# Performance work log

Hardware: AMD Instinct MI355X
Metric: run time of the kernel (lower is better)

## Reference

```python
import jax, jax.numpy as jnp
import numpy as np
from jax import lax

EPS = 1e-5
SLOPE = 0.01  # default leaky_relu negative slope

def _conv1d(x, w):
    # x: [B, Cin, L], w: [Cout, Cin, K]; padding=1 (same for K=3)
    return lax.conv_general_dilated(x, w, window_strides=(1,), padding=[(1, 1)],
                                    dimension_numbers=('NCH', 'OIH', 'NCH'))

def _bn_train(x, gamma, beta, axes):
    # training-mode BatchNorm: batch stats over `axes`, biased variance
    mean = jnp.mean(x, axis=axes, keepdims=True)
    var = jnp.mean(jnp.square(x - mean), axis=axes, keepdims=True)
    shape = [1] * x.ndim
    shape[1] = x.shape[1]
    g = gamma.reshape(shape); b = beta.reshape(shape)
    return (x - mean) * g / jnp.sqrt(var + EPS) + b

def setup_inputs() -> dict:
    key = jax.random.key(0)
    ks = jax.random.split(key, 6)
    d, d2, out_dim = 64, 128, 128
    bs, T, N = 16, 32, 256
    s = 0.05
    return {
        'x': jax.random.normal(ks[0], (bs, T, N, d), jnp.float32),
        'conv1_w': jax.random.normal(ks[1], (d2, d, 3), jnp.float32) * s,
        'bn1_g': jnp.ones((d2,), jnp.float32), 'bn1_b': jnp.zeros((d2,), jnp.float32),
        'conv2_w': jax.random.normal(ks[2], (d2, d2, 3), jnp.float32) * s,
        'bn2_g': jnp.ones((d2,), jnp.float32), 'bn2_b': jnp.zeros((d2,), jnp.float32),
        'map_w': jax.random.normal(ks[3], (d2, d2), jnp.float32) * s,
        'map_b': jnp.zeros((d2,), jnp.float32),
        'theta_w': jax.random.normal(ks[4], (out_dim, d2), jnp.float32) * s,
        'theta_b': jnp.zeros((out_dim,), jnp.float32),
        'bnS_g': jnp.ones((out_dim,), jnp.float32), 'bnS_b': jnp.zeros((out_dim,), jnp.float32),
    }

def reference(x, conv1_w, bn1_g, bn1_b, conv2_w, bn2_g, bn2_b,
              map_w, map_b, theta_w, theta_b, bnS_g, bnS_b):
    bs, T, N, d = x.shape
    d2 = 2 * d
    # ---- Temporal 1D CNN over time, per node ----
    tem = jnp.transpose(x, (0, 2, 1, 3)).reshape(bs * N, T, d)      # [BN, T, d]
    h = jnp.transpose(tem, (0, 2, 1))                               # [BN, d, T]
    h = jax.nn.relu(_bn_train(_conv1d(h, conv1_w), bn1_g, bn1_b, (0, 2)))
    h = jax.nn.relu(_bn_train(_conv1d(h, conv2_w), bn2_g, bn2_b, (0, 2)))  # [BN, 2d, T]
    # faithful raw reshape (mixes channel/time layout exactly like the torch code)
    tem_out = h.reshape(bs, N, T, d2)
    spa = jnp.transpose(tem_out, (0, 2, 1, 3)).reshape(bs * T, N, d2)  # [B', N, 2d]
    # ---- Dot-product graph construction ----
    mapped = jnp.einsum('bnd,ed->bne', spa, map_w) + map_b            # Linear(2d,2d)
    adj = jnp.einsum('bnd,bmd->bnm', mapped, mapped)                  # [B', N, N]
    eye = jnp.eye(N, dtype=adj.dtype)
    adj = jax.nn.leaky_relu(adj - eye * 1e8, SLOPE)
    adj = jax.nn.softmax(adj, axis=-1) + eye
    # ---- MPNN (k=1): theta(A @ X), BN over channels, leaky_relu ----
    agg = jnp.einsum('bnm,bmd->bnd', adj, spa)                        # bmm(A, X)
    out = jnp.einsum('bnd,od->bno', agg, theta_w) + theta_b           # [B', N, out]
    out = jnp.transpose(out, (0, 2, 1))                               # [B', out, N]
    out = _bn_train(out, bnS_g, bnS_b, (0, 2))
    out = jnp.transpose(out, (0, 2, 1))
    return jax.nn.leaky_relu(out, SLOPE)
```

## Files before the change

### kernel.cpp

```cpp
#include <hip/hip_runtime.h>

#define SLOPE 0.01f
#define EPSB 1e-5f
#define INV_CNT (1.0f/131072.0f)

typedef unsigned short u16;
typedef unsigned int u32;
typedef __attribute__((ext_vector_type(8))) short s16x8;
typedef __attribute__((ext_vector_type(4))) float f4;

__device__ float g_stats[3][2][128];
__device__ float g_sb[3][2][128];
__device__ float g_part[2048][256];
__device__ u16 g_w1h[3][128][64];
__device__ u16 g_w1l[3][128][64];
__device__ u16 g_w2h[3][128][128];
__device__ u16 g_w2l[3][128][128];
__device__ u16 g_wmh[128][128];
__device__ u16 g_wml[128][128];
__device__ u16 g_wqh[128][128];
__device__ u16 g_wql[128][128];

__device__ __forceinline__ float lrelu(float x){ return x > 0.f ? x : SLOPE*x; }
__device__ __forceinline__ u16 f2b(float f){
  u32 u = __float_as_uint(f);
  return (u16)((u + 0x7fffu + ((u >> 16) & 1u)) >> 16);
}
__device__ __forceinline__ float b2f(u16 h){ return __uint_as_float(((u32)h) << 16); }
__device__ __forceinline__ u32 pk(float a, float b){ return (u32)f2b(a) | ((u32)f2b(b) << 16); }
__device__ __forceinline__ u32 pkhl(float f){
  u16 h = f2b(f);
  u16 l = f2b(f - b2f(h));
  return (u32)h | ((u32)l << 16);
}
__device__ __forceinline__ float unhl(u32 v){ return b2f((u16)(v & 0xffff)) + b2f((u16)(v >> 16)); }

__global__ void k_zero(){
  int i = blockIdx.x*256 + threadIdx.x;
  if (i < 768) ((float*)g_stats)[i] = 0.f;
}

__global__ void k_reduce(int which){
  const float* base = &g_part[blockIdx.x*128][0];
  int j = threadIdx.x;
  float s = 0.f;
  #pragma unroll 4
  for (int r = 0; r < 128; ++r) s += base[r*256 + j];
  atomicAdd(&((float*)g_stats)[which*256 + j], s);
}

__global__ void k_prepw(const float* __restrict__ w1, const float* __restrict__ w2,
                        const float* __restrict__ mapw, const float* __restrict__ thw){
  int idx = blockIdx.x*256 + threadIdx.x;
  if (idx < 24576){
    int kk = idx >> 13, r = idx & 8191, co = r >> 6, ci = r & 63;
    float v = w1[co*192 + ci*3 + kk];
    u16 h = f2b(v);
    g_w1h[kk][co][ci] = h; g_w1l[kk][co][ci] = f2b(v - b2f(h));
  } else if (idx < 73728){
    int j = idx - 24576;
    int kk = j >> 14, r = j & 16383, co = r >> 7, ci = r & 127;
    float v = w2[co*384 + ci*3 + kk];
    u16 h = f2b(v);
    g_w2h[kk][co][ci] = h; g_w2l[kk][co][ci] = f2b(v - b2f(h));
  } else if (idx < 90112){
    int j = idx - 73728;
    float v = mapw[j];
    u16 h = f2b(v);
    ((u16*)g_wmh)[j] = h; ((u16*)g_wml)[j] = f2b(v - b2f(h));
  } else if (idx < 106496){
    int j = idx - 90112;
    float v = thw[j];
    u16 h = f2b(v);
    ((u16*)g_wqh)[j] = h; ((u16*)g_wql)[j] = f2b(v - b2f(h));
  }
}

__global__ void k_finalize(const float* __restrict__ g, const float* __restrict__ bta, int which){
  int c = threadIdx.x;
  float mean = g_stats[which][0][c] * INV_CNT;
  float var  = g_stats[which][1][c] * INV_CNT - mean*mean;
  float sc = g[c] * rsqrtf(var + EPSB);
  g_sb[which][0][c] = sc;
  g_sb[which][1][c] = bta[c] - mean*sc;
}

__global__ __launch_bounds__(256, 4) void k_conv1(const float* __restrict__ x, u16* __restrict__ y1hl){
  __shared__ __align__(16) u16 a0h[2][34][72];
  __shared__ __align__(16) u16 a0l[2][34][72];
  const int bid = blockIdx.x;
  const int bn0 = bid*2;
  const int b = bn0 >> 8, n = bn0 & 255;
  const int tid = threadIdx.x;
  const int w = tid >> 6, l = tid & 63, quad = l >> 4, lm = l & 15;
  f4 acc[2][4];
  #pragma unroll
  for (int i = 0; i < 2; ++i)
    #pragma unroll
    for (int j = 0; j < 4; ++j) acc[i][j] = (f4)0.f;

  {
    int nn = tid >> 7, rem = tid & 127, t = rem >> 2, ci0 = (rem & 3)*16;
    const float* px = x + ((b*32 + t)*256 + n + nn)*64 + ci0;
    u16 hh[16], ll[16];
    #pragma unroll
    for (int j = 0; j < 4; ++j){
      float4 v = *(const float4*)(px + 4*j);
      float vv[4] = {v.x, v.y, v.z, v.w};
      #pragma unroll
      for (int e = 0; e < 4; ++e){
        u16 h = f2b(vv[e]);
        hh[4*j+e] = h; ll[4*j+e] = f2b(vv[e] - b2f(h));
      }
    }
    *(uint4*)&a0h[nn][t+1][ci0]   = *(uint4*)&hh[0];
    *(uint4*)&a0h[nn][t+1][ci0+8] = *(uint4*)&hh[8];
    *(uint4*)&a0l[nn][t+1][ci0]   = *(uint4*)&ll[0];
    *(uint4*)&a0l[nn][t+1][ci0+8] = *(uint4*)&ll[8];
  }
  for (int u = tid; u < 288; u += 256){
    int a = u / 144, rr = u % 144, r = rr / 36, cw = rr % 36;
    u32* base = a ? (u32*)&a0l[r>>1][(r&1)*33][0] : (u32*)&a0h[r>>1][(r&1)*33][0];
    base[cw] = 0u;
  }
  __syncthreads();

  for (int kk = 0; kk < 3; ++kk){
    #pragma unroll
    for (int s = 0; s < 2; ++s){
      int ci0 = s*32 + quad*8;
      s16x8 wh[2], wl[2], bh[4], bl[4];
      #pragma unroll
      for (int i = 0; i < 2; ++i){
        wh[i] = *(const s16x8*)&g_w1h[kk][(2*w+i)*16 + lm][ci0];
        wl[i] = *(const s16x8*)&g_w1l[kk][(2*w+i)*16 + lm][ci0];
      }
      #pragma unroll
      for (int nt = 0; nt < 4; ++nt){
        bh[nt] = *(s16x8*)&a0h[nt>>1][(nt&1)*16 + lm + kk][ci0];
        bl[nt] = *(s16x8*)&a0l[nt>>1][(nt&1)*16 + lm + kk][ci0];
      }
      #pragma unroll
      for (int i = 0; i < 2; ++i)
        #pragma unroll
        for (int nt = 0; nt < 4; ++nt){
          acc[i][nt] = __builtin_amdgcn_mfma_f32_16x16x32_bf16(wh[i], bh[nt], acc[i][nt], 0, 0, 0);
          acc[i][nt] = __builtin_amdgcn_mfma_f32_16x16x32_bf16(wh[i], bl[nt], acc[i][nt], 0, 0, 0);
          acc[i][nt] = __builtin_amdgcn_mfma_f32_16x16x32_bf16(wl[i], bh[nt], acc[i][nt], 0, 0, 0);
        }
    }
  }
  #pragma unroll
  for (int i = 0; i < 2; ++i){
    int co0 = (2*w+i)*16 + quad*4;
    float s0=0,s1=0,s2=0,s3=0,q0=0,q1=0,q2=0,q3=0;
    #pragma unroll
    for (int nt = 0; nt < 4; ++nt){
      f4 a = acc[i][nt];
      int nn = nt >> 1, t = (nt & 1)*16 + lm;
      uint4 p;
      p.x = pkhl(a.x); p.y = pkhl(a.y); p.z = pkhl(a.z); p.w = pkhl(a.w);
      *(uint4*)&y1hl[(((bn0+nn)*32 + t)*128 + co0)*2] = p;
      s0+=a.x; s1+=a.y; s2+=a.z; s3+=a.w;
      q0+=a.x*a.x; q1+=a.y*a.y; q2+=a.z*a.z; q3+=a.w*a.w;
    }
    #pragma unroll
    for (int m = 1; m < 16; m <<= 1){
      s0+=__shfl_xor(s0,m); s1+=__shfl_xor(s1,m); s2+=__shfl_xor(s2,m); s3+=__shfl_xor(s3,m);
      q0+=__shfl_xor(q0,m); q1+=__shfl_xor(q1,m); q2+=__shfl_xor(q2,m); q3+=__shfl_xor(q3,m);
    }
    if (lm == 0){
      f4 sv = {s0,s1,s2,s3}, qv = {q0,q1,q2,q3};
      *(f4*)&g_part[bid][co0]       = sv;
      *(f4*)&g_part[bid][128 + co0] = qv;
    }
  }
}

__global__ __launch_bounds__(256, 4) void k_conv2(const u16* __restrict__ y1hl, u16* __restrict__ spa){
  __shared__ __align__(16) u16 a1s[2][34][136];
  const int bid = blockIdx.x;
  const int bn0 = bid*2;
  const int b = bn0 >> 8, n = bn0 & 255;
  const int tid = threadIdx.x;
  const int w = tid >> 6, l = tid & 63, quad = l >> 4, lm = l & 15;
  f4 acc2[4][2];
  #pragma unroll
  for (int mt = 0; mt < 4; ++mt)
    #pragma unroll
    for (int i = 0; i < 2; ++i) acc2[mt][i] = (f4)0.f;

  {
    int nn = tid >> 7, rem = tid & 127, t = rem >> 2, ci0 = (rem & 3)*32;
    const u16* py = y1hl + (((bn0+nn)*32 + t)*128)*2;
    #pragma unroll
    for (int j = 0; j < 4; ++j){
      uint4 va = *(const uint4*)&py[(ci0 + 8*j)*2];
      uint4 vb = *(const uint4*)&py[(ci0 + 8*j + 4)*2];
      u32 vv[8] = {va.x, va.y, va.z, va.w, vb.x, vb.y, vb.z, vb.w};
      u16 oo[8];
      #pragma unroll
      for (int e = 0; e < 8; ++e){
        int ci = ci0 + 8*j + e;
        float f = fmaxf(fmaf(unhl(vv[e]), g_sb[0][0][ci], g_sb[0][1][ci]), 0.f);
        oo[e] = f2b(f);
      }
      *(uint4*)&a1s[nn][t+1][ci0 + 8*j] = *(uint4*)&oo[0];
    }
  }
  for (int u = tid; u < 272; u += 256){
    int r = u/68, cw = u%68;
    ((u32*)&a1s[r>>1][(r&1)*33][0])[cw] = 0u;
  }
  __syncthreads();

  for (int kk = 0; kk < 3; ++kk){
    #pragma unroll
    for (int s = 0; s < 4; ++s){
      int ci0 = s*32 + quad*8;
      s16x8 ax[4], bwh[2], bwl[2];
      #pragma unroll
      for (int i = 0; i < 2; ++i){
        bwh[i] = *(const s16x8*)&g_w2h[kk][(2*w+i)*16 + lm][ci0];
        bwl[i] = *(const s16x8*)&g_w2l[kk][(2*w+i)*16 + lm][ci0];
      }
      #pragma unroll
      for (int mt = 0; mt < 4; ++mt) ax[mt] = *(s16x8*)&a1s[mt>>1][(mt&1)*16 + lm + kk][ci0];
      #pragma unroll
      for (int mt = 0; mt < 4; ++mt)
        #pragma unroll
        for (int i = 0; i < 2; ++i){
          acc2[mt][i] = __builtin_amdgcn_mfma_f32_16x16x32_bf16(ax[mt], bwh[i], acc2[mt][i], 0, 0, 0);
          acc2[mt][i] = __builtin_amdgcn_mfma_f32_16x16x32_bf16(ax[mt], bwl[i], acc2[mt][i], 0, 0, 0);
        }
    }
  }
  #pragma unroll
  for (int i = 0; i < 2; ++i){
    int co = (2*w+i)*16 + lm;
    float s = 0.f, q = 0.f;
    #pragma unroll
    for (int mt = 0; mt < 4; ++mt){
      f4 a = acc2[mt][i];
      int off0 = co*32 + (mt&1)*16 + quad*4;
      int tp = off0 >> 7, cp = off0 & 127;
      int row = (b*32 + tp)*256 + (n + (mt>>1));
      uint2 p; p.x = pk(a.x, a.y); p.y = pk(a.z, a.w);
      *(uint2*)&spa[row*128 + cp] = p;
      s += a.x + a.y + a.z + a.w;
      q += a.x*a.x + a.y*a.y + a.z*a.z + a.w*a.w;
    }
    s += __shfl_xor(s, 16); s += __shfl_xor(s, 32);
    q += __shfl_xor(q, 16); q += __shfl_xor(q, 32);
    if (l < 16){
      g_part[bid][co]       = s;
      g_part[bid][128 + co] = q;
    }
  }
}

__global__ __launch_bounds__(256, 4) void k_gemm128b(const u16* A,
                                                     u16* spaw,
                                                     const float* __restrict__ bvec,
                                                     void* __restrict__ outv,
                                                     int wsel, int do_stats){
  __shared__ __align__(16) u16 As[64][136];
  const u16* Wh = wsel ? &g_wqh[0][0] : &g_wmh[0][0];
  const u16* Wl = wsel ? &g_wql[0][0] : &g_wml[0][0];
  const int bid = blockIdx.x;
  const int rowbase = bid * 64;
  const int tid = threadIdx.x;
  const int w = tid >> 6, l = tid & 63, quad = l >> 4, lm = l & 15;
  f4 acc[2][4];
  #pragma unroll
  for (int i = 0; i < 2; ++i)
    #pragma unroll
    for (int rt = 0; rt < 4; ++rt) acc[i][rt] = (f4)0.f;

  { int r = tid >> 2, c0 = (tid & 3)*32;
    int row = rowbase + r;
    if (wsel == 0){
      int c = ((row >> 8) & 31)*4 + (tid & 3);
      float sc = g_sb[1][0][c], bi = g_sb[1][1][c];
      #pragma unroll
      for (int j = 0; j < 4; ++j){
        uint4 v = *(const uint4*)&A[row*128 + c0 + 8*j];
        u32 vv[4] = {v.x, v.y, v.z, v.w};
        u16 oo[8];
        #pragma unroll
        for (int e = 0; e < 4; ++e){
          oo[2*e]   = f2b(fmaxf(fmaf(b2f((u16)(vv[e] & 0xffff)), sc, bi), 0.f));
          oo[2*e+1] = f2b(fmaxf(fmaf(b2f((u16)(vv[e] >> 16)),    sc, bi), 0.f));
        }
        uint4 ov = *(uint4*)&oo[0];
        *(uint4*)&As[r][c0 + 8*j] = ov;
        *(uint4*)&spaw[row*128 + c0 + 8*j] = ov;
      }
    } else {
      #pragma unroll
      for (int j = 0; j < 4; ++j)
        *(uint4*)&As[r][c0 + 8*j] = *(const uint4*)&A[row*128 + c0 + 8*j];
    }
  }
  __syncthreads();

  #pragma unroll
  for (int s = 0; s < 4; ++s){
    int k0 = s*32 + quad*8;
    s16x8 awh[2], awl[2], ba[4];
    #pragma unroll
    for (int i = 0; i < 2; ++i){
      awh[i] = *(const s16x8*)&Wh[((2*w+i)*16 + lm)*128 + k0];
      awl[i] = *(const s16x8*)&Wl[((2*w+i)*16 + lm)*128 + k0];
    }
    #pragma unroll
    for (int rt = 0; rt < 4; ++rt) ba[rt] = *(s16x8*)&As[rt*16 + lm][k0];
    #pragma unroll
    for (int i = 0; i < 2; ++i)
      #pragma unroll
      for (int rt = 0; rt < 4; ++rt){
        acc[i][rt] = __builtin_amdgcn_mfma_f32_16x16x32_bf16(awh[i], ba[rt], acc[i][rt], 0, 0, 0);
        acc[i][rt] = __builtin_amdgcn_mfma_f32_16x16x32_bf16(awl[i], ba[rt], acc[i][rt], 0, 0, 0);
      }
  }
  #pragma unroll
  for (int i = 0; i < 2; ++i){
    int e0 = (2*w+i)*16 + quad*4;
    f4 bv = *(const f4*)&bvec[e0];
    if (wsel == 0){
      u16* mh = (u16*)outv;
      u16* ml = mh + 16777216;
      int dc = e0 >> 5, ec = e0 & 31;
      #pragma unroll
      for (int rt = 0; rt < 4; ++rt){
        int row = rowbase + rt*16 + lm;
        int bp = row >> 8, m = row & 255;
        f4 o = acc[i][rt] + bv;
        float fv[4] = {o.x, o.y, o.z, o.w};
        u16 hh[4], ll[4];
        #pragma unroll
        for (int e = 0; e < 4; ++e){
          u16 h = f2b(fv[e]);
          hh[e] = h; ll[e] = f2b(fv[e] - b2f(h));
        }
        int off = ((bp*4 + dc)*256 + m)*32 + ec;
        *(uint2*)&mh[off] = *(uint2*)&hh[0];
        *(uint2*)&ml[off] = *(uint2*)&ll[0];
      }
    } else {
      float* outp = (float*)outv;
      f4 sv = (f4)0.f, qv = (f4)0.f;
      #pragma unroll
      for (int rt = 0; rt < 4; ++rt){
        int row = rowbase + rt*16 + lm;
        f4 o = acc[i][rt] + bv;
        *(f4*)&outp[row*128 + e0] = o;
        sv += o; qv += o*o;
      }
      if (do_stats){
        #pragma unroll
        for (int m = 1; m < 16; m <<= 1){
          sv.x+=__shfl_xor(sv.x,m); sv.y+=__shfl_xor(sv.y,m); sv.z+=__shfl_xor(sv.z,m); sv.w+=__shfl_xor(sv.w,m);
          qv.x+=__shfl_xor(qv.x,m); qv.y+=__shfl_xor(qv.y,m); qv.z+=__shfl_xor(qv.z,m); qv.w+=__shfl_xor(qv.w,m);
        }
        if (lm == 0){
          *(f4*)&g_part[bid][e0]       = sv;
          *(f4*)&g_part[bid][128 + e0] = qv;
        }
      }
    }
  }
}

__global__ __launch_bounds__(256) void k_adjagg(const u16* __restrict__ mh,
                                                const u16* __restrict__ ml,
                                                const u16* __restrict__ spa,
                                                u16* __restrict__ agg){
  __shared__ __align__(16) char smem[52224];
  u16 (*mbh)[40]   = (u16(*)[40])(smem);
  u16 (*mbl)[40]   = (u16(*)[40])(smem + 20480);
  u16 (*Ps)[264]   = (u16(*)[264])(smem);
  u16 (*spasT)[72] = (u16(*)[72])(smem + 33792);
  const int rb = blockIdx.x;
  const int vb = (rb & 7)*256 + (rb >> 3);
  const int bp = vb >> 2;
  const int nt = vb & 3;
  const int tid = threadIdx.x;
  const int w = tid >> 6, l = tid & 63, quad = l >> 4, lm = l & 15;

  f4 sacc[16];
  #pragma unroll
  for (int ct = 0; ct < 16; ++ct) sacc[ct] = (f4)0.f;

  for (int dc = 0; dc < 4; ++dc){
    __syncthreads();
    {
      const u16* srch = mh + ((bp*4 + dc) << 13);
      const u16* srcl = ml + ((bp*4 + dc) << 13);
      int m0 = tid >> 2, seg = (tid & 3)*8;
      #pragma unroll
      for (int r = 0; r < 4; ++r){
        int m = m0 + r*64;
        *(uint4*)&mbh[m][seg] = *(const uint4*)&srch[m*32 + seg];
        *(uint4*)&mbl[m][seg] = *(const uint4*)&srcl[m*32 + seg];
      }
    }
    __syncthreads();
    s16x8 amh = *(s16x8*)&mbh[nt*64 + w*16 + lm][quad*8];
    s16x8 aml = *(s16x8*)&mbl[nt*64 + w*16 + lm][quad*8];
    #pragma unroll
    for (int ct = 0; ct < 16; ++ct){
      s16x8 bmh = *(s16x8*)&mbh[ct*16 + lm][quad*8];
      s16x8 bml = *(s16x8*)&mbl[ct*16 + lm][quad*8];
      sacc[ct] = __builtin_amdgcn_mfma_f32_16x16x32_bf16(amh, bmh, sacc[ct], 0, 0, 0);
      sacc[ct] = __builtin_amdgcn_mfma_f32_16x16x32_bf16(amh, bml, sacc[ct], 0, 0, 0);
      sacc[ct] = __builtin_amdgcn_mfma_f32_16x16x32_bf16(aml, bmh, sacc[ct], 0, 0, 0);
    }
  }
  __syncthreads();

  #pragma unroll
  for (int r = 0; r < 4; ++r){
    int rowg = nt*64 + w*16 + quad*4 + r;
    float v[16]; float mx = -3.0e38f;
    #pragma unroll
    for (int ct = 0; ct < 16; ++ct){
      float t = sacc[ct][r];
      if (ct*16 + lm == rowg) t -= 1e8f;
      t = lrelu(t);
      v[ct] = t; mx = fmaxf(mx, t);
    }
    #pragma unroll
    for (int m = 1; m < 16; m <<= 1) mx = fmaxf(mx, __shfl_xor(mx, m));
    float sum = 0.f;
    #pragma unroll
    for (int ct = 0; ct < 16; ++ct){ float e = __expf(v[ct] - mx); v[ct] = e; sum += e; }
    #pragma unroll
    for (int m = 1; m < 16; m <<= 1) sum += __shfl_xor(sum, m);
    float inv = 1.0f / sum;
    #pragma unroll
    for (int ct = 0; ct < 16; ++ct)
      Ps[w*16 + quad*4 + r][ct*16 + lm] = f2b(v[ct] * inv);
  }

  f4 acc2[2][4];
  #pragma unroll
  for (int i = 0; i < 2; ++i)
    #pragma unroll
    for (int rt = 0; rt < 4; ++rt) acc2[i][rt] = (f4)0.f;

  for (int mc2 = 0; mc2 < 4; ++mc2){
    __syncthreads();
    {
      int mlo = tid & 63;
      int db = (tid >> 6)*8;
      const u16* ps = spa + (bp*256 + mc2*64 + mlo)*128;
      #pragma unroll
      for (int r = 0; r < 4; ++r){
        int d0 = db + r*32;
        uint4 v = *(const uint4*)(ps + d0);
        u16 h[8]; *(uint4*)&h[0] = v;
        #pragma unroll
        for (int j = 0; j < 8; ++j) spasT[d0+j][mlo] = h[j];
      }
    }
    __syncthreads();
    #pragma unroll
    for (int ks = 0; ks < 2; ++ks){
      int m0 = ks*32 + quad*8;
      s16x8 afs[2], bfp[4];
      #pragma unroll
      for (int i = 0; i < 2; ++i) afs[i] = *(s16x8*)&spasT[(2*w+i)*16 + lm][m0];
      #pragma unroll
      for (int rt = 0; rt < 4; ++rt) bfp[rt] = *(s16x8*)&Ps[rt*16 + lm][mc2*64 + m0];
      #pragma unroll
      for (int i = 0; i < 2; ++i)
        #pragma unroll
        for (int rt = 0; rt < 4; ++rt)
          acc2[i][rt] = __builtin_amdgcn_mfma_f32_16x16x32_bf16(afs[i], bfp[rt], acc2[i][rt], 0, 0, 0);
    }
  }
  #pragma unroll
  for (int i = 0; i < 2; ++i){
    int d0 = (2*w+i)*16 + quad*4;
    #pragma unroll
    for (int rt = 0; rt < 4; ++rt){
      int grow = bp*256 + nt*64 + rt*16 + lm;
      uint2 sp = *(const uint2*)&spa[grow*128 + d0];
      f4 a = acc2[i][rt];
      a.x += b2f((u16)(sp.x & 0xffff)); a.y += b2f((u16)(sp.x >> 16));
      a.z += b2f((u16)(sp.y & 0xffff)); a.w += b2f((u16)(sp.y >> 16));
      uint2 p; p.x = pk(a.x, a.y); p.y = pk(a.z, a.w);
      *(uint2*)&agg[grow*128 + d0] = p;
    }
  }
}

__global__ void k_bnout(float* __restrict__ outp){
  int idx = blockIdx.x*256 + threadIdx.x;
  int flat = idx*4;
  int o = flat & 127;
  float4 v = *(const float4*)(outp + flat);
  v.x = lrelu(fmaf(v.x, g_sb[2][0][o+0], g_sb[2][1][o+0]));
  v.y = lrelu(fmaf(v.y, g_sb[2][0][o+1], g_sb[2][1][o+1]));
  v.z = lrelu(fmaf(v.z, g_sb[2][0][o+2], g_sb[2][1][o+2]));
  v.w = lrelu(fmaf(v.w, g_sb[2][0][o+3], g_sb[2][1][o+3]));
  *(float4*)(outp + flat) = v;
}

extern "C" void kernel_launch(void* const* d_in, const int* in_sizes, int n_in,
                              void* d_out, int out_size, void* d_ws, size_t ws_size,
                              hipStream_t stream) {
  const float* x    = (const float*)d_in[0];
  const float* w1   = (const float*)d_in[1];
  const float* bn1g = (const float*)d_in[2];
  const float* bn1b = (const float*)d_in[3];
  const float* w2   = (const float*)d_in[4];
  const float* bn2g = (const float*)d_in[5];
  const float* bn2b = (const float*)d_in[6];
  const float* mapw = (const float*)d_in[7];
  const float* mapb = (const float*)d_in[8];
  const float* thw  = (const float*)d_in[9];
  const float* thb  = (const float*)d_in[10];
  const float* bnSg = (const float*)d_in[11];
  const float* bnSb = (const float*)d_in[12];
  float* outp = (float*)d_out;

  u16* spa = (u16*)d_ws;
  u16* agg = spa + 16777216;

  u16* y1hl = (u16*)d_out;
  u16* mh   = (u16*)d_out;
  u16* ml   = mh + 16777216;

  k_zero<<<3, 256, 0, stream>>>();
  k_prepw<<<416, 256, 0, stream>>>(w1, w2, mapw, thw);
  k_conv1<<<2048, 256, 0, stream>>>(x, y1hl);
  k_reduce<<<16, 256, 0, stream>>>(0);
  k_finalize<<<1, 128, 0, stream>>>(bn1g, bn1b, 0);
  k_conv2<<<2048, 256, 0, stream>>>(y1hl, spa);
  k_reduce<<<16, 256, 0, stream>>>(1);
  k_finalize<<<1, 128, 0, stream>>>(bn2g, bn2b, 1);
  k_gemm128b<<<2048, 256, 0, stream>>>(spa, spa, mapb, (void*)mh, 0, 0);
  k_adjagg<<<2048, 256, 0, stream>>>(mh, ml, spa, agg);
  k_gemm128b<<<2048, 256, 0, stream>>>(agg, agg, thb, (void*)outp, 1, 1);
  k_reduce<<<16, 256, 0, stream>>>(2);
  k_finalize<<<1, 128, 0, stream>>>(bnSg, bnSb, 2);
  k_bnout<<<16384, 256, 0, stream>>>(outp);
}
```

Before: 406.2 us.

## Fuse BN reductions with finalize, store conv1 output as fp32, pretranspose spa

Folds k_zero into k_prepw and merges k_finalize into k_reduce with a last-block counter, removing four kernel launches. Conv1 now writes plain fp32 instead of packed hi/lo bf16 pairs, which keeps the same byte count but drops the split and recombine arithmetic. The mapping GEMM also writes a transposed copy of spa into a global buffer, so adjagg can load spasT with vector copies instead of doing an element-wise transpose in shared memory. The cost is an extra 32 MB scattered 2-byte write in the GEMM.

```diff
diff --git a/kernel.cpp b/kernel.cpp
--- a/kernel.cpp
+++ b/kernel.cpp
@@ -12,6 +12,7 @@
 __device__ float g_stats[3][2][128];
 __device__ float g_sb[3][2][128];
 __device__ float g_part[2048][256];
+__device__ int   g_cnt[3];
 __device__ u16 g_w1h[3][128][64];
 __device__ u16 g_w1l[3][128][64];
 __device__ u16 g_w2h[3][128][128];
@@ -20,6 +21,7 @@
 __device__ u16 g_wml[128][128];
 __device__ u16 g_wqh[128][128];
 __device__ u16 g_wql[128][128];
+__device__ u16 g_sT[16777216];
 
 __device__ __forceinline__ float lrelu(float x){ return x > 0.f ? x : SLOPE*x; }
 __device__ __forceinline__ u16 f2b(float f){
@@ -28,30 +30,12 @@
 }
 __device__ __forceinline__ float b2f(u16 h){ return __uint_as_float(((u32)h) << 16); }
 __device__ __forceinline__ u32 pk(float a, float b){ return (u32)f2b(a) | ((u32)f2b(b) << 16); }
-__device__ __forceinline__ u32 pkhl(float f){
-  u16 h = f2b(f);
-  u16 l = f2b(f - b2f(h));
-  return (u32)h | ((u32)l << 16);
-}
-__device__ __forceinline__ float unhl(u32 v){ return b2f((u16)(v & 0xffff)) + b2f((u16)(v >> 16)); }
-
-__global__ void k_zero(){
-  int i = blockIdx.x*256 + threadIdx.x;
-  if (i < 768) ((float*)g_stats)[i] = 0.f;
-}
-
-__global__ void k_reduce(int which){
-  const float* base = &g_part[blockIdx.x*128][0];
-  int j = threadIdx.x;
-  float s = 0.f;
-  #pragma unroll 4
-  for (int r = 0; r < 128; ++r) s += base[r*256 + j];
-  atomicAdd(&((float*)g_stats)[which*256 + j], s);
-}
 
 __global__ void k_prepw(const float* __restrict__ w1, const float* __restrict__ w2,
                         const float* __restrict__ mapw, const float* __restrict__ thw){
   int idx = blockIdx.x*256 + threadIdx.x;
+  if (idx < 768) ((float*)g_stats)[idx] = 0.f;
+  if (idx < 3) g_cnt[idx] = 0;
   if (idx < 24576){
     int kk = idx >> 13, r = idx & 8191, co = r >> 6, ci = r & 63;
     float v = w1[co*192 + ci*3 + kk];
@@ -76,16 +60,33 @@
   }
 }
 
-__global__ void k_finalize(const float* __restrict__ g, const float* __restrict__ bta, int which){
-  int c = threadIdx.x;
-  float mean = g_stats[which][0][c] * INV_CNT;
-  float var  = g_stats[which][1][c] * INV_CNT - mean*mean;
-  float sc = g[c] * rsqrtf(var + EPSB);
-  g_sb[which][0][c] = sc;
-  g_sb[which][1][c] = bta[c] - mean*sc;
-}
-
-__global__ __launch_bounds__(256, 4) void k_conv1(const float* __restrict__ x, u16* __restrict__ y1hl){
+__global__ void k_reduce(const float* __restrict__ g, const float* __restrict__ bta, int which){
+  const float* base = &g_part[blockIdx.x*128][0];
+  int j = threadIdx.x;
+  float s = 0.f;
+  #pragma unroll 4
+  for (int r = 0; r < 128; ++r) s += base[r*256 + j];
+  atomicAdd(&((float*)g_stats)[which*256 + j], s);
+  __threadfence();
+  __shared__ int lastf;
+  __syncthreads();
+  if (threadIdx.x == 0) lastf = (atomicAdd(&g_cnt[which], 1) == 15) ? 1 : 0;
+  __syncthreads();
+  if (lastf){
+    __threadfence();
+    if (j < 128){
+      float sm = atomicAdd(&g_stats[which][0][j], 0.f);
+      float sq = atomicAdd(&g_stats[which][1][j], 0.f);
+      float mean = sm * INV_CNT;
+      float var  = sq * INV_CNT - mean*mean;
+      float sc = g[j] * rsqrtf(var + EPSB);
+      g_sb[which][0][j] = sc;
+      g_sb[which][1][j] = bta[j] - mean*sc;
+    }
+  }
+}
+
+__global__ __launch_bounds__(256, 4) void k_conv1(const float* __restrict__ x, float* __restrict__ y1f){
   __shared__ __align__(16) u16 a0h[2][34][72];
   __shared__ __align__(16) u16 a0l[2][34][72];
   const int bid = blockIdx.x;
@@ -158,9 +159,7 @@
     for (int nt = 0; nt < 4; ++nt){
       f4 a = acc[i][nt];
       int nn = nt >> 1, t = (nt & 1)*16 + lm;
-      uint4 p;
-      p.x = pkhl(a.x); p.y = pkhl(a.y); p.z = pkhl(a.z); p.w = pkhl(a.w);
-      *(uint4*)&y1hl[(((bn0+nn)*32 + t)*128 + co0)*2] = p;
+      *(f4*)&y1f[((bn0+nn)*32 + t)*128 + co0] = a;
       s0+=a.x; s1+=a.y; s2+=a.z; s3+=a.w;
       q0+=a.x*a.x; q1+=a.y*a.y; q2+=a.z*a.z; q3+=a.w*a.w;
     }
@@ -177,7 +176,7 @@
   }
 }
 
-__global__ __launch_bounds__(256, 4) void k_conv2(const u16* __restrict__ y1hl, u16* __restrict__ spa){
+__global__ __launch_bounds__(256, 4) void k_conv2(const float* __restrict__ y1f, u16* __restrict__ spa){
   __shared__ __align__(16) u16 a1s[2][34][136];
   const int bid = blockIdx.x;
   const int bn0 = bid*2;
@@ -192,18 +191,17 @@
 
   {
     int nn = tid >> 7, rem = tid & 127, t = rem >> 2, ci0 = (rem & 3)*32;
-    const u16* py = y1hl + (((bn0+nn)*32 + t)*128)*2;
+    const float* py = y1f + ((bn0+nn)*32 + t)*128;
     #pragma unroll
     for (int j = 0; j < 4; ++j){
-      uint4 va = *(const uint4*)&py[(ci0 + 8*j)*2];
-      uint4 vb = *(const uint4*)&py[(ci0 + 8*j + 4)*2];
-      u32 vv[8] = {va.x, va.y, va.z, va.w, vb.x, vb.y, vb.z, vb.w};
+      float4 v1 = *(const float4*)(py + ci0 + 8*j);
+      float4 v2 = *(const float4*)(py + ci0 + 8*j + 4);
+      float vv[8] = {v1.x, v1.y, v1.z, v1.w, v2.x, v2.y, v2.z, v2.w};
       u16 oo[8];
       #pragma unroll
       for (int e = 0; e < 8; ++e){
         int ci = ci0 + 8*j + e;
-        float f = fmaxf(fmaf(unhl(vv[e]), g_sb[0][0][ci], g_sb[0][1][ci]), 0.f);
-        oo[e] = f2b(f);
+        oo[e] = f2b(fmaxf(fmaf(vv[e], g_sb[0][0][ci], g_sb[0][1][ci]), 0.f));
       }
       *(uint4*)&a1s[nn][t+1][ci0 + 8*j] = *(uint4*)&oo[0];
     }
@@ -282,6 +280,8 @@
     if (wsel == 0){
       int c = ((row >> 8) & 31)*4 + (tid & 3);
       float sc = g_sb[1][0][c], bi = g_sb[1][1][c];
+      int mrel = row & 63;
+      u16* st = g_sT + (((row >> 6) * 128) << 6);
       #pragma unroll
       for (int j = 0; j < 4; ++j){
         uint4 v = *(const uint4*)&A[row*128 + c0 + 8*j];
@@ -295,6 +295,9 @@
         uint4 ov = *(uint4*)&oo[0];
         *(uint4*)&As[r][c0 + 8*j] = ov;
         *(uint4*)&spaw[row*128 + c0 + 8*j] = ov;
+        #pragma unroll
+        for (int e = 0; e < 8; ++e)
+          st[(c0 + 8*j + e)*64 + mrel] = oo[e];
       }
     } else {
       #pragma unroll
@@ -452,17 +455,12 @@
   for (int mc2 = 0; mc2 < 4; ++mc2){
     __syncthreads();
     {
-      int mlo = tid & 63;
-      int db = (tid >> 6)*8;
-      const u16* ps = spa + (bp*256 + mc2*64 + mlo)*128;
-      #pragma unroll
-      for (int r = 0; r < 4; ++r){
-        int d0 = db + r*32;
-        uint4 v = *(const uint4*)(ps + d0);
-        u16 h[8]; *(uint4*)&h[0] = v;
-        #pragma unroll
-        for (int j = 0; j < 8; ++j) spasT[d0+j][mlo] = h[j];
-      }
+      const u16* src = g_sT + (((bp*4 + mc2)*128) << 6) + (tid >> 1)*64 + (tid & 1)*32;
+      u16* dst = &spasT[tid >> 1][(tid & 1)*32];
+      *(uint4*)(dst)      = *(const uint4*)(src);
+      *(uint4*)(dst + 8)  = *(const uint4*)(src + 8);
+      *(uint4*)(dst + 16) = *(const uint4*)(src + 16);
+      *(uint4*)(dst + 24) = *(const uint4*)(src + 24);
     }
     __syncthreads();
     #pragma unroll
@@ -529,22 +527,17 @@
   u16* spa = (u16*)d_ws;
   u16* agg = spa + 16777216;
 
-  u16* y1hl = (u16*)d_out;
-  u16* mh   = (u16*)d_out;
-  u16* ml   = mh + 16777216;
-
-  k_zero<<<3, 256, 0, stream>>>();
+  float* y1f = (float*)d_out;
+  u16* mh    = (u16*)d_out;
+
   k_prepw<<<416, 256, 0, stream>>>(w1, w2, mapw, thw);
-  k_conv1<<<2048, 256, 0, stream>>>(x, y1hl);
-  k_reduce<<<16, 256, 0, stream>>>(0);
-  k_finalize<<<1, 128, 0, stream>>>(bn1g, bn1b, 0);
-  k_conv2<<<2048, 256, 0, stream>>>(y1hl, spa);
-  k_reduce<<<16, 256, 0, stream>>>(1);
-  k_finalize<<<1, 128, 0, stream>>>(bn2g, bn2b, 1);
+  k_conv1<<<2048, 256, 0, stream>>>(x, y1f);
+  k_reduce<<<16, 256, 0, stream>>>(bn1g, bn1b, 0);
+  k_conv2<<<2048, 256, 0, stream>>>(y1f, spa);
+  k_reduce<<<16, 256, 0, stream>>>(bn2g, bn2b, 1);
   k_gemm128b<<<2048, 256, 0, stream>>>(spa, spa, mapb, (void*)mh, 0, 0);
-  k_adjagg<<<2048, 256, 0, stream>>>(mh, ml, spa, agg);
+  k_adjagg<<<2048, 256, 0, stream>>>(mh, mh + 16777216, spa, agg);
   k_gemm128b<<<2048, 256, 0, stream>>>(agg, agg, thb, (void*)outp, 1, 1);
-  k_reduce<<<16, 256, 0, stream>>>(2);
-  k_finalize<<<1, 128, 0, stream>>>(bnSg, bnSb, 2);
+  k_reduce<<<16, 256, 0, stream>>>(bnSg, bnSb, 2);
   k_bnout<<<16384, 256, 0, stream>>>(outp);
 }
```

Result: no change. 407.5 us (+0.3%).
